# Performance work log

Measured on AMD Instinct MI355X. Metric: run time of the kernel, lower is better.

## Reference

```python
import jax, jax.numpy as jnp
import numpy as np

# NF4 codebook (bitsandbytes nf4 quant_type), 16 levels in [-1, 1]
NF4 = jnp.array([
    -1.0, -0.6961928009986877, -0.5250730514526367, -0.39491748809814453,
    -0.28444138169288635, -0.18477343022823334, -0.09105003625154495, 0.0,
    0.07958029955625534, 0.16093020141124725, 0.24611230194568634,
    0.33791524171829224, 0.44070982933044434, 0.5626170039176941,
    0.7229568362236023, 1.0], dtype=jnp.float32)
BLOCK = 64  # bitsandbytes default quant block size

TOKENS, HD, M = 8192, 4096, 11008


def dequant_nf4(codes, scales):
    # codes: [out, in] int in [0,16); scales: [out, in//BLOCK] per-block absmax
    out_f, in_f = codes.shape
    w = NF4[codes].reshape(out_f, in_f // BLOCK, BLOCK) * scales[:, :, None]
    return w.reshape(out_f, in_f)


def setup_inputs() -> dict:
    key = jax.random.key(0)
    k = jax.random.split(key, 7)
    return {
        "x": jax.random.normal(k[0], (TOKENS, HD), dtype=jnp.float32),
        "gate_codes": jax.random.randint(k[1], (M, HD), 0, 16, dtype=jnp.int32),
        "gate_scales": jax.random.uniform(k[2], (M, HD // BLOCK), dtype=jnp.float32) * 0.1,
        "up_codes": jax.random.randint(k[3], (M, HD), 0, 16, dtype=jnp.int32),
        "up_scales": jax.random.uniform(k[4], (M, HD // BLOCK), dtype=jnp.float32) * 0.1,
        "down_codes": jax.random.randint(k[5], (HD, M), 0, 16, dtype=jnp.int32),
        "down_scales": jax.random.uniform(k[6], (HD, M // BLOCK), dtype=jnp.float32) * 0.1,
    }


def reference(x, gate_codes, gate_scales, up_codes, up_scales, down_codes, down_scales):
    Wg = dequant_nf4(gate_codes, gate_scales)   # [m, hd]
    Wu = dequant_nf4(up_codes, up_scales)       # [m, hd]
    Wd = dequant_nf4(down_codes, down_scales)   # [hd, m]
    g = jnp.einsum('td,md->tm', x, Wg)          # gate_proj(x)
    u = jnp.einsum('td,md->tm', x, Wu)          # up_proj(x)
    h = jax.nn.silu(g) * u                      # SwiGLU
    return jnp.einsum('tm,dm->td', h, Wd)       # down_proj
```

## Files before the change

### kernel.cpp

```cpp
#include <hip/hip_runtime.h>
#include <hip/hip_bf16.h>

typedef _Float16 half8 __attribute__((ext_vector_type(8)));
typedef float floatx4 __attribute__((ext_vector_type(4)));

__device__ __constant__ float NF4_TAB[16] = {
    -1.0f, -0.6961928009986877f, -0.5250730514526367f, -0.39491748809814453f,
    -0.28444138169288635f, -0.18477343022823334f, -0.09105003625154495f, 0.0f,
    0.07958029955625534f, 0.16093020141124725f, 0.24611230194568634f,
    0.33791524171829224f, 0.44070982933044434f, 0.5626170039176941f,
    0.7229568362236023f, 1.0f};

typedef __attribute__((address_space(3))) void lds_t;
typedef __attribute__((address_space(1))) void gbl_t;

__device__ __forceinline__ void gload16(const void* g, void* l) {
  __builtin_amdgcn_global_load_lds((gbl_t*)g, (lds_t*)l, 16, 0, 0);
}

#define FENCE() asm volatile("" ::: "memory")

__global__ void cvt_f32_to_f16(const float* __restrict__ in,
                               _Float16* __restrict__ out, int total8) {
  int stride = gridDim.x * blockDim.x;
  for (int i = blockIdx.x * blockDim.x + threadIdx.x; i < total8; i += stride) {
    long e = (long)i * 8;
    const float4* ip = reinterpret_cast<const float4*>(in + e);
    float4 a = ip[0], b = ip[1];
    half8 o;
    o[0] = (_Float16)a.x; o[1] = (_Float16)a.y;
    o[2] = (_Float16)a.z; o[3] = (_Float16)a.w;
    o[4] = (_Float16)b.x; o[5] = (_Float16)b.y;
    o[6] = (_Float16)b.z; o[7] = (_Float16)b.w;
    *reinterpret_cast<half8*>(out + e) = o;
  }
}

__global__ void dequant_nf4(const int* __restrict__ codes,
                            const float* __restrict__ scales,
                            _Float16* __restrict__ out,
                            int total8, int C, int CB) {
  __shared__ float lut[16];
  if (threadIdx.x < 16) lut[threadIdx.x] = NF4_TAB[threadIdx.x];
  __syncthreads();
  int stride = gridDim.x * blockDim.x;
  for (int i = blockIdx.x * blockDim.x + threadIdx.x; i < total8; i += stride) {
    long e = (long)i * 8;
    int row = (int)(e / C);
    int col = (int)(e - (long)row * C);
    float sc = scales[row * CB + (col >> 6)];
    const int4* cp = reinterpret_cast<const int4*>(codes + e);
    int4 c0 = cp[0];
    int4 c1 = cp[1];
    half8 o;
    o[0] = (_Float16)(lut[c0.x & 15] * sc);
    o[1] = (_Float16)(lut[c0.y & 15] * sc);
    o[2] = (_Float16)(lut[c0.z & 15] * sc);
    o[3] = (_Float16)(lut[c0.w & 15] * sc);
    o[4] = (_Float16)(lut[c1.x & 15] * sc);
    o[5] = (_Float16)(lut[c1.y & 15] * sc);
    o[6] = (_Float16)(lut[c1.z & 15] * sc);
    o[7] = (_Float16)(lut[c1.w & 15] * sc);
    *reinterpret_cast<half8*>(out + e) = o;
  }
}

template <int K, int N, int EPI>
__global__ __launch_bounds__(512, 2) void gemm256(
    const _Float16* __restrict__ A,
    const _Float16* __restrict__ B,
    _Float16* __restrict__ GH,
    float* __restrict__ OUT) {
  constexpr int NT = K / 64;
  constexpr int NBC = N / 256;
  __shared__ __align__(16) _Float16 lds[2 * 32768];

  const int t = threadIdx.x;
  const int lane = t & 63;
  const int wave = t >> 6;
  const int wm = wave >> 2;
  const int wn = wave & 3;

  const int xcd = blockIdx.x & 7;
  const int j = blockIdx.x >> 3;
  const int bm = 4 * xcd + (j & 3);
  const int bn = j >> 2;

  const int lc = (t & 3) ^ ((t >> 3) & 3);
  const _Float16* gA = A + ((long)bm * 256 + (t >> 2)) * K + lc * 8;
  const _Float16* gB = B + ((long)bn * 256 + (t >> 2)) * K + lc * 8;
  const long rstep = (long)128 * K;
  const int dst = t * 8;

  const int rA = wm * 128 + (lane & 15);
  const int rB = wn * 64 + (lane & 15);
  const int ckA = ((lane >> 4) ^ ((rA >> 1) & 3)) * 8;
  const int ckB = ((lane >> 4) ^ ((rB >> 1) & 3)) * 8;
  const int offA = rA * 32 + ckA;
  const int offB = 16384 + rB * 32 + ckB;

#define STAGE_SLOT(gp, slab, koff, dbuf)                                   \
  gload16((gp) + (koff), lds + (dbuf) * 32768 + (slab) + dst);             \
  gload16((gp) + (koff) + rstep, lds + (dbuf) * 32768 + (slab) + dst + 4096);

  STAGE_SLOT(gA, 0, 0, 0);
  STAGE_SLOT(gB, 16384, 0, 0);
  STAGE_SLOT(gA, 8192, 32, 0);
  STAGE_SLOT(gB, 24576, 32, 0);
  gA += 64; gB += 64;
  asm volatile("s_waitcnt vmcnt(4)" ::: "memory");
  __builtin_amdgcn_s_barrier();
  FENCE();

  floatx4 acc[8][4] = {};

  for (int kt = 0; kt < NT; ++kt) {
    const int cb = kt & 1;
    const int sbuf = cb ^ 1;
    const _Float16* lb = lds + cb * 32768;
    const bool st = (kt + 1 < NT);
    const bool last = (kt == NT - 1);

    half8 a[8], b[2];

#pragma unroll
    for (int i = 0; i < 8; ++i)
      a[i] = *reinterpret_cast<const half8*>(&lb[offA + i * 512]);
    b[0] = *reinterpret_cast<const half8*>(&lb[offB]);
    b[1] = *reinterpret_cast<const half8*>(&lb[offB + 512]);
    if (st) { STAGE_SLOT(gA, 0, 0, sbuf); }
    __builtin_amdgcn_s_barrier();
    FENCE();
    __builtin_amdgcn_s_setprio(1);
#pragma unroll
    for (int i = 0; i < 8; ++i) {
      acc[i][0] = __builtin_amdgcn_mfma_f32_16x16x32_f16(a[i], b[0], acc[i][0], 0, 0, 0);
      acc[i][1] = __builtin_amdgcn_mfma_f32_16x16x32_f16(a[i], b[1], acc[i][1], 0, 0, 0);
    }
    __builtin_amdgcn_s_setprio(0);
    __builtin_amdgcn_s_barrier();
    FENCE();

    b[0] = *reinterpret_cast<const half8*>(&lb[offB + 2 * 512]);
    b[1] = *reinterpret_cast<const half8*>(&lb[offB + 3 * 512]);
    if (st) { STAGE_SLOT(gB, 16384, 0, sbuf); }
    if (last) { asm volatile("s_waitcnt vmcnt(0)" ::: "memory"); }
    else      { asm volatile("s_waitcnt vmcnt(4)" ::: "memory"); }
    __builtin_amdgcn_s_barrier();
    FENCE();
    __builtin_amdgcn_s_setprio(1);
#pragma unroll
    for (int i = 0; i < 8; ++i) {
      acc[i][2] = __builtin_amdgcn_mfma_f32_16x16x32_f16(a[i], b[0], acc[i][2], 0, 0, 0);
      acc[i][3] = __builtin_amdgcn_mfma_f32_16x16x32_f16(a[i], b[1], acc[i][3], 0, 0, 0);
    }
    __builtin_amdgcn_s_setprio(0);
    __builtin_amdgcn_s_barrier();
    FENCE();

#pragma unroll
    for (int i = 0; i < 8; ++i)
      a[i] = *reinterpret_cast<const half8*>(&lb[8192 + offA + i * 512]);
    b[0] = *reinterpret_cast<const half8*>(&lb[8192 + offB]);
    b[1] = *reinterpret_cast<const half8*>(&lb[8192 + offB + 512]);
    if (st) { STAGE_SLOT(gA, 8192, 32, sbuf); }
    __builtin_amdgcn_s_barrier();
    FENCE();
    __builtin_amdgcn_s_setprio(1);
#pragma unroll
    for (int i = 0; i < 8; ++i) {
      acc[i][0] = __builtin_amdgcn_mfma_f32_16x16x32_f16(a[i], b[0], acc[i][0], 0, 0, 0);
      acc[i][1] = __builtin_amdgcn_mfma_f32_16x16x32_f16(a[i], b[1], acc[i][1], 0, 0, 0);
    }
    __builtin_amdgcn_s_setprio(0);
    __builtin_amdgcn_s_barrier();
    FENCE();

    b[0] = *reinterpret_cast<const half8*>(&lb[8192 + offB + 2 * 512]);
    b[1] = *reinterpret_cast<const half8*>(&lb[8192 + offB + 3 * 512]);
    if (st) { STAGE_SLOT(gB, 24576, 32, sbuf); gA += 64; gB += 64; }
    if (!last) { asm volatile("s_waitcnt vmcnt(4)" ::: "memory"); }
    __builtin_amdgcn_s_barrier();
    FENCE();
    __builtin_amdgcn_s_setprio(1);
#pragma unroll
    for (int i = 0; i < 8; ++i) {
      acc[i][2] = __builtin_amdgcn_mfma_f32_16x16x32_f16(a[i], b[0], acc[i][2], 0, 0, 0);
      acc[i][3] = __builtin_amdgcn_mfma_f32_16x16x32_f16(a[i], b[1], acc[i][3], 0, 0, 0);
    }
    __builtin_amdgcn_s_setprio(0);
    __builtin_amdgcn_s_barrier();
    FENCE();
  }
#undef STAGE_SLOT

  const int r0 = bm * 256 + wm * 128 + (lane >> 4) * 4;
  const int c0 = bn * 256 + wn * 64 + (lane & 15);

  if (EPI == 1) {
    _Float16* lg = lds;
    const _Float16* gsrc = GH + (long)(bm * 256) * N + bn * 256;
#pragma unroll
    for (int r = 0; r < 16; ++r) {
      const int row = r * 16 + (t >> 5);
      const int col = (t & 31) * 8;
      gload16(gsrc + (long)row * N + col, lg + r * 4096 + t * 8);
    }
    asm volatile("s_waitcnt vmcnt(0)" ::: "memory");
    __builtin_amdgcn_s_barrier();
    FENCE();
    const int lr0 = wm * 128 + (lane >> 4) * 4;
    const int lc0 = wn * 64 + (lane & 15);
#pragma unroll
    for (int i = 0; i < 8; ++i) {
#pragma unroll
      for (int j2 = 0; j2 < 4; ++j2) {
#pragma unroll
        for (int ii = 0; ii < 4; ++ii) {
          const long idx = (long)(r0 + i * 16 + ii) * N + (c0 + j2 * 16);
          float u = acc[i][j2][ii];
          float g = (float)lg[(lr0 + i * 16 + ii) * 256 + (lc0 + j2 * 16)];
          GH[idx] = (_Float16)(g / (1.0f + __expf(-g)) * u);
        }
      }
    }
  } else {
#pragma unroll
    for (int i = 0; i < 8; ++i) {
#pragma unroll
      for (int j2 = 0; j2 < 4; ++j2) {
#pragma unroll
        for (int ii = 0; ii < 4; ++ii) {
          const long idx = (long)(r0 + i * 16 + ii) * N + (c0 + j2 * 16);
          if (EPI == 0) {
            GH[idx] = (_Float16)acc[i][j2][ii];
          } else {
            OUT[idx] = acc[i][j2][ii];
          }
        }
      }
    }
  }
}

extern "C" void kernel_launch(void* const* d_in, const int* in_sizes, int n_in,
                              void* d_out, int out_size, void* d_ws, size_t ws_size,
                              hipStream_t stream) {
  const float* x           = (const float*)d_in[0];
  const int*   gate_codes  = (const int*)d_in[1];
  const float* gate_scales = (const float*)d_in[2];
  const int*   up_codes    = (const int*)d_in[3];
  const float* up_scales   = (const float*)d_in[4];
  const int*   down_codes  = (const int*)d_in[5];
  const float* down_scales = (const float*)d_in[6];
  float* out = (float*)d_out;

  const long T = 8192, HD = 4096, M = 11008;

  char* ws = (char*)d_ws;
  _Float16* x16 = (_Float16*)ws;
  _Float16* W   = (_Float16*)(ws + T * HD * 2);
  _Float16* gh  = (_Float16*)(ws + T * HD * 2 + M * HD * 2);

  cvt_f32_to_f16<<<2048, 256, 0, stream>>>(x, x16, (int)(T * HD / 8));

  dequant_nf4<<<2048, 256, 0, stream>>>(gate_codes, gate_scales, W,
                                        (int)(M * HD / 8), (int)HD, (int)(HD / 64));
  gemm256<4096, 11008, 0><<<(8192 / 256) * (11008 / 256), 512, 0, stream>>>(
      x16, W, gh, nullptr);

  dequant_nf4<<<2048, 256, 0, stream>>>(up_codes, up_scales, W,
                                        (int)(M * HD / 8), (int)HD, (int)(HD / 64));
  gemm256<4096, 11008, 1><<<(8192 / 256) * (11008 / 256), 512, 0, stream>>>(
      x16, W, gh, nullptr);

  dequant_nf4<<<2048, 256, 0, stream>>>(down_codes, down_scales, W,
                                        (int)(HD * M / 8), (int)M, (int)(M / 64));
  gemm256<11008, 4096, 2><<<(8192 / 256) * (4096 / 256), 512, 0, stream>>>(
      gh, W, nullptr, out);
}
```

Before: 2.228 ms.

## Add 256x128 triple-buffered GEMM kernel for gate and up projections

Adds a new GEMM kernel for the gate and up projections with a 256x128 output tile, a K step of 32 and a three-slot LDS ring buffer, launched with occupancy hint 4 instead of 2. The two large GEMMs now use it, which doubles the grid size and is meant to improve wave occupancy, reduce tail effects (11008/256 is not an integer) and hide load latency with a deeper pipeline. The original 256x256 kernel is kept only for the down projection, and its unused SwiGLU epilogue is removed. The trade-off is less reuse of each A tile per block, so more global and LDS traffic per FLOP, and more barriers per K step.

```diff
diff --git a/kernel.cpp b/kernel.cpp
--- a/kernel.cpp
+++ b/kernel.cpp
@@ -66,6 +66,144 @@
 }
 
 template <int K, int N, int EPI>
+__global__ __launch_bounds__(512, 4) void gemm256x128(
+    const _Float16* __restrict__ A,
+    const _Float16* __restrict__ B,
+    _Float16* __restrict__ GH) {
+  constexpr int NT = K / 32;
+  constexpr int NBC = N / 128;
+  __shared__ __align__(16) _Float16 lds[3 * 12288];
+
+  const int t = threadIdx.x;
+  const int lane = t & 63;
+  const int wave = t >> 6;
+  const int wm = wave >> 2;
+  const int wn = wave & 3;
+
+  const int xcd = blockIdx.x & 7;
+  const int j = blockIdx.x >> 3;
+  const int bm = 4 * xcd + (j & 3);
+  const int bn = j >> 2;
+
+  const int lc = (t & 3) ^ ((t >> 3) & 3);
+  const _Float16* gA = A + ((long)bm * 256 + (t >> 2)) * K + lc * 8;
+  const _Float16* gB = B + ((long)bn * 128 + (t >> 2)) * K + lc * 8;
+  const long rstep = (long)128 * K;
+  const int dst = t * 8;
+
+  const int rA = wm * 128 + (lane & 15);
+  const int rB = wn * 32 + (lane & 15);
+  const int ckA = ((lane >> 4) ^ ((rA >> 1) & 3)) * 8;
+  const int ckB = ((lane >> 4) ^ ((rB >> 1) & 3)) * 8;
+  const int offA = rA * 32 + ckA;
+  const int offB = 8192 + rB * 32 + ckB;
+
+#define STAGE_A(dbuf) \
+  gload16(gA, lds + (dbuf) * 12288 + dst); \
+  gload16(gA + rstep, lds + (dbuf) * 12288 + dst + 4096); gA += 32;
+#define STAGE_B(dbuf) \
+  gload16(gB, lds + (dbuf) * 12288 + 8192 + dst); gB += 32;
+
+  STAGE_A(0); STAGE_B(0);
+  STAGE_A(1); STAGE_B(1);
+  asm volatile("s_waitcnt vmcnt(3)" ::: "memory");
+  __builtin_amdgcn_s_barrier();
+  FENCE();
+
+  floatx4 acc[8][2] = {};
+
+  for (int kt = 0; kt < NT; ++kt) {
+    const _Float16* lb = lds + (kt % 3) * 12288;
+    const int s2 = (kt + 2) % 3;
+    const bool st = (kt + 2 < NT);
+
+    half8 a[4], b[2];
+
+#pragma unroll
+    for (int i = 0; i < 4; ++i)
+      a[i] = *reinterpret_cast<const half8*>(&lb[offA + i * 512]);
+    b[0] = *reinterpret_cast<const half8*>(&lb[offB]);
+    b[1] = *reinterpret_cast<const half8*>(&lb[offB + 512]);
+    if (st) { STAGE_A(s2); }
+    __builtin_amdgcn_s_barrier();
+    FENCE();
+    __builtin_amdgcn_s_setprio(1);
+#pragma unroll
+    for (int i = 0; i < 4; ++i) {
+      acc[i][0] = __builtin_amdgcn_mfma_f32_16x16x32_f16(a[i], b[0], acc[i][0], 0, 0, 0);
+      acc[i][1] = __builtin_amdgcn_mfma_f32_16x16x32_f16(a[i], b[1], acc[i][1], 0, 0, 0);
+    }
+    __builtin_amdgcn_s_setprio(0);
+    __builtin_amdgcn_s_barrier();
+    FENCE();
+
+#pragma unroll
+    for (int i = 0; i < 4; ++i)
+      a[i] = *reinterpret_cast<const half8*>(&lb[offA + (4 + i) * 512]);
+    if (st) { STAGE_B(s2); }
+    if (kt < NT - 2)       { asm volatile("s_waitcnt vmcnt(3)" ::: "memory"); }
+    else if (kt == NT - 2) { asm volatile("s_waitcnt vmcnt(0)" ::: "memory"); }
+    __builtin_amdgcn_s_barrier();
+    FENCE();
+    __builtin_amdgcn_s_setprio(1);
+#pragma unroll
+    for (int i = 0; i < 4; ++i) {
+      acc[4 + i][0] = __builtin_amdgcn_mfma_f32_16x16x32_f16(a[i], b[0], acc[4 + i][0], 0, 0, 0);
+      acc[4 + i][1] = __builtin_amdgcn_mfma_f32_16x16x32_f16(a[i], b[1], acc[4 + i][1], 0, 0, 0);
+    }
+    __builtin_amdgcn_s_setprio(0);
+    __builtin_amdgcn_s_barrier();
+    FENCE();
+  }
+#undef STAGE_A
+#undef STAGE_B
+
+  const int r0 = bm * 256 + wm * 128 + (lane >> 4) * 4;
+  const int c0 = bn * 128 + wn * 32 + (lane & 15);
+
+  if (EPI == 1) {
+    _Float16* lg = lds;
+    const _Float16* gsrc = GH + (long)(bm * 256) * N + bn * 128;
+#pragma unroll
+    for (int r = 0; r < 8; ++r) {
+      const int row = r * 32 + (t >> 4);
+      const int col = (t & 15) * 8;
+      gload16(gsrc + (long)row * N + col, lg + r * 4096 + t * 8);
+    }
+    asm volatile("s_waitcnt vmcnt(0)" ::: "memory");
+    __builtin_amdgcn_s_barrier();
+    FENCE();
+    const int lr0 = wm * 128 + (lane >> 4) * 4;
+    const int lc0 = wn * 32 + (lane & 15);
+#pragma unroll
+    for (int i = 0; i < 8; ++i) {
+#pragma unroll
+      for (int j2 = 0; j2 < 2; ++j2) {
+#pragma unroll
+        for (int ii = 0; ii < 4; ++ii) {
+          const long idx = (long)(r0 + i * 16 + ii) * N + (c0 + j2 * 16);
+          float u = acc[i][j2][ii];
+          float g = (float)lg[(lr0 + i * 16 + ii) * 128 + (lc0 + j2 * 16)];
+          GH[idx] = (_Float16)(g / (1.0f + __expf(-g)) * u);
+        }
+      }
+    }
+  } else {
+#pragma unroll
+    for (int i = 0; i < 8; ++i) {
+#pragma unroll
+      for (int j2 = 0; j2 < 2; ++j2) {
+#pragma unroll
+        for (int ii = 0; ii < 4; ++ii) {
+          const long idx = (long)(r0 + i * 16 + ii) * N + (c0 + j2 * 16);
+          GH[idx] = (_Float16)acc[i][j2][ii];
+        }
+      }
+    }
+  }
+}
+
+template <int K, int N, int EPI>
 __global__ __launch_bounds__(512, 2) void gemm256(
     const _Float16* __restrict__ A,
     const _Float16* __restrict__ B,
@@ -196,47 +334,17 @@
 
   const int r0 = bm * 256 + wm * 128 + (lane >> 4) * 4;
   const int c0 = bn * 256 + wn * 64 + (lane & 15);
-
-  if (EPI == 1) {
-    _Float16* lg = lds;
-    const _Float16* gsrc = GH + (long)(bm * 256) * N + bn * 256;
-#pragma unroll
-    for (int r = 0; r < 16; ++r) {
-      const int row = r * 16 + (t >> 5);
-      const int col = (t & 31) * 8;
-      gload16(gsrc + (long)row * N + col, lg + r * 4096 + t * 8);
-    }
-    asm volatile("s_waitcnt vmcnt(0)" ::: "memory");
-    __builtin_amdgcn_s_barrier();
-    FENCE();
-    const int lr0 = wm * 128 + (lane >> 4) * 4;
-    const int lc0 = wn * 64 + (lane & 15);
-#pragma unroll
-    for (int i = 0; i < 8; ++i) {
-#pragma unroll
-      for (int j2 = 0; j2 < 4; ++j2) {
-#pragma unroll
-        for (int ii = 0; ii < 4; ++ii) {
-          const long idx = (long)(r0 + i * 16 + ii) * N + (c0 + j2 * 16);
-          float u = acc[i][j2][ii];
-          float g = (float)lg[(lr0 + i * 16 + ii) * 256 + (lc0 + j2 * 16)];
-          GH[idx] = (_Float16)(g / (1.0f + __expf(-g)) * u);
-        }
-      }
-    }
-  } else {
-#pragma unroll
-    for (int i = 0; i < 8; ++i) {
-#pragma unroll
-      for (int j2 = 0; j2 < 4; ++j2) {
-#pragma unroll
-        for (int ii = 0; ii < 4; ++ii) {
-          const long idx = (long)(r0 + i * 16 + ii) * N + (c0 + j2 * 16);
-          if (EPI == 0) {
-            GH[idx] = (_Float16)acc[i][j2][ii];
-          } else {
-            OUT[idx] = acc[i][j2][ii];
-          }
+#pragma unroll
+  for (int i = 0; i < 8; ++i) {
+#pragma unroll
+    for (int j2 = 0; j2 < 4; ++j2) {
+#pragma unroll
+      for (int ii = 0; ii < 4; ++ii) {
+        const long idx = (long)(r0 + i * 16 + ii) * N + (c0 + j2 * 16);
+        if (EPI == 0) {
+          GH[idx] = (_Float16)acc[i][j2][ii];
+        } else {
+          OUT[idx] = acc[i][j2][ii];
         }
       }
     }
@@ -266,13 +374,13 @@
 
   dequant_nf4<<<2048, 256, 0, stream>>>(gate_codes, gate_scales, W,
                                         (int)(M * HD / 8), (int)HD, (int)(HD / 64));
-  gemm256<4096, 11008, 0><<<(8192 / 256) * (11008 / 256), 512, 0, stream>>>(
-      x16, W, gh, nullptr);
+  gemm256x128<4096, 11008, 0><<<(8192 / 256) * (11008 / 128), 512, 0, stream>>>(
+      x16, W, gh);
 
   dequant_nf4<<<2048, 256, 0, stream>>>(up_codes, up_scales, W,
                                         (int)(M * HD / 8), (int)HD, (int)(HD / 64));
-  gemm256<4096, 11008, 1><<<(8192 / 256) * (11008 / 256), 512, 0, stream>>>(
-      x16, W, gh, nullptr);
+  gemm256x128<4096, 11008, 1><<<(8192 / 256) * (11008 / 128), 512, 0, stream>>>(
+      x16, W, gh);
 
   dequant_nf4<<<2048, 256, 0, stream>>>(down_codes, down_scales, W,
                                         (int)(HD * M / 8), (int)M, (int)(M / 64));
```

Result: slower. 2.323 ms (+4.3%).
